# Kernel optimization log

Measured on AMD Instinct MI355X. Metric: run time of the kernel, lower is better.

Reference implementation:

```python
import jax, jax.numpy as jnp
from jax import lax
import numpy as np

BATCH = 8
INPUT_LEN = 768
OUTPUT_LEN = 192
MULTISCALE = (1, 2, 4)
HIDDEN = 256          # HiPPO order N == spectral channels
MODES = 32            # min(32, min(output_len, input_len)//2)
NUM_FEAT = 64


def hippo_matrices(N, dt):
    """HiPPO-LegT continuous matrices, bilinear-discretized (scipy cont2discrete equiv)."""
    Q = np.arange(N, dtype=np.float64)
    R = (2 * Q + 1)[:, None]
    j, i = np.meshgrid(Q, Q)
    A = np.where(i < j, -1.0, (-1.0) ** (i - j + 1)) * R
    B = ((-1.0) ** Q[:, None]) * R  # [N,1]
    I = np.eye(N)
    ima = I - (dt / 2.0) * A
    Ad = np.linalg.solve(ima, I + (dt / 2.0) * A)
    Bd = np.linalg.solve(ima, B * dt).squeeze(-1)
    return Ad.astype(np.float32), Bd.astype(np.float32)


def legendre_eval_matrix(N, dt):
    """eval_matrix[t, n] = P_n(1 - 2*vals[t]), vals = arange(0,1,dt)."""
    vals = np.arange(0.0, 1.0, dt)
    x = 1.0 - 2.0 * vals
    P = np.zeros((N, len(vals)), dtype=np.float64)
    P[0] = 1.0
    if N > 1:
        P[1] = x
    for n in range(1, N - 1):
        P[n + 1] = ((2 * n + 1) * x * P[n] - n * P[n - 1]) / (n + 1)
    return P.T.astype(np.float32)  # [len(vals), N]


def setup_inputs() -> dict:
    key = jax.random.key(0)
    k1, k2, k3, k4 = jax.random.split(key, 4)
    scale = 1.0 / (HIDDEN * HIDDEN)
    return {
        "inputs": jax.random.normal(k1, (BATCH, INPUT_LEN, NUM_FEAT), jnp.float32),
        "spec_wr": scale * jax.random.uniform(k2, (3, HIDDEN, HIDDEN, MODES), jnp.float32),
        "spec_wi": scale * jax.random.uniform(k3, (3, HIDDEN, HIDDEN, MODES), jnp.float32),
        "mlp_w": 0.1 * jax.random.normal(k4, (1, 3), jnp.float32),
        "mlp_b": jnp.zeros((1,), jnp.float32),
    }


def _film_forward(inputs, spec_wr, spec_wi, mlp_w, mlp_b):
    B_, _, D = inputs.shape
    preds = []
    for idx, scale in enumerate(MULTISCALE):
        dt = 1.0 / OUTPUT_LEN / scale
        Ad_np, Bd_np = hippo_matrices(HIDDEN, dt)
        em_np = legendre_eval_matrix(HIDDEN, dt)[-OUTPUT_LEN:]  # [out_len, N]
        Ad = jnp.asarray(Ad_np)
        Bd = jnp.asarray(Bd_np)
        em = jnp.asarray(em_np)
        T = scale * OUTPUT_LEN
        # HiPPO recurrence: c_t = c_{t-1} @ A^T + f_t * B  (sequential scan over time)
        f = jnp.transpose(inputs[:, -T:], (1, 0, 2))  # [T, B, D]

        def step(c, f_t, Ad=Ad, Bd=Bd):
            c = c @ Ad.T + f_t[..., None] * Bd
            return c, c

        c0 = jnp.zeros((B_, D, HIDDEN), inputs.dtype)
        _, cs = lax.scan(step, c0, f)               # [T, B, D, N]
        x = jnp.transpose(cs, (1, 2, 3, 0))          # [B, D, N, T]
        # SpectralConv1d: rfft -> complex mixing on low modes -> irfft
        x_ft = jnp.fft.rfft(x)                       # [B, D, N, T//2+1]
        w = (spec_wr[idx] + 1j * spec_wi[idx]).astype(jnp.complex64)  # [N, N, modes]
        out_m = jnp.einsum('bjix,iox->bjox', x_ft[..., :MODES], w)    # [B, D, N, modes]
        nfreq = T // 2 + 1
        out_ft = jnp.concatenate(
            [out_m, jnp.zeros(out_m.shape[:-1] + (nfreq - MODES,), out_m.dtype)], axis=-1)
        x = jnp.fft.irfft(out_ft, n=T)               # [B, D, N, T]
        # input_len >= output_len -> pick time index output_len-1, then project with Legendre
        x_out = x[:, :, :, OUTPUT_LEN - 1]           # [B, D, N]
        preds.append(x_out @ em.T)                   # [B, D, out_len]
    pred = jnp.stack(preds, axis=-1)                 # [B, D, out_len, 3]
    pred = jnp.squeeze(pred @ mlp_w.T + mlp_b, -1)   # [B, D, out_len]
    return jnp.transpose(pred, (0, 2, 1))            # [B, out_len, D]


def reference(inputs, spec_wr, spec_wi, mlp_w, mlp_b):
    return _film_forward(inputs, spec_wr, spec_wi, mlp_w, mlp_b)
```

## Files before the change

### kernel.cpp

```cpp
#include <hip/hip_runtime.h>


#define OFF_MF64  0
#define OFF_YA    1572864
#define OFF_YB    3145728
#define OFF_Z     4718592
#define OFF_F     7864320
#define OFF_PIV   8650752
#define OFF_FLAG  8653824
#define OFF_AP0   10223616
#define OFF_AP1   11010048
#define OFF_BD    11796480
#define OFF_V     11800576
#define OFF_EM    14159872
#define OFF_P     14749696
#define OFF_K     16125952
#define OFF_U4    29298688
#define OFF_WT4   117440512
#define OFF_C32   167772160
#define OFF_SEG4  211812352

typedef _Float16 half8 __attribute__((ext_vector_type(8)));
typedef float f32x4 __attribute__((ext_vector_type(4)));

__device__ __forceinline__ double a_entry(int i, int j){
  double base = (i < j) ? -1.0 : (((i - j) & 1) ? 1.0 : -1.0);
  return base * (double)(2*i + 1);
}

__device__ __forceinline__ unsigned int dpp_umax(unsigned int x){
  unsigned int t;
  t = (unsigned int)__builtin_amdgcn_update_dpp((int)x, (int)x, 0x111, 0xF, 0xF, false); x = x > t ? x : t;
  t = (unsigned int)__builtin_amdgcn_update_dpp((int)x, (int)x, 0x112, 0xF, 0xF, false); x = x > t ? x : t;
  t = (unsigned int)__builtin_amdgcn_update_dpp((int)x, (int)x, 0x114, 0xF, 0xE, false); x = x > t ? x : t;
  t = (unsigned int)__builtin_amdgcn_update_dpp((int)x, (int)x, 0x118, 0xF, 0xC, false); x = x > t ? x : t;
  t = (unsigned int)__builtin_amdgcn_update_dpp((int)x, (int)x, 0x142, 0xA, 0xF, false); x = x > t ? x : t;
  t = (unsigned int)__builtin_amdgcn_update_dpp((int)x, (int)x, 0x143, 0xC, 0xF, false); x = x > t ? x : t;
  return x;
}

__global__ void k_init(double* __restrict__ Mf64, float* __restrict__ em,
                       int* __restrict__ flags){
  int s = blockIdx.y, i = blockIdx.x, j = threadIdx.x;
  if (i < 256){
    double dt = (1.0 / 192.0) / (double)(1 << s);
    double m = ((i == j) ? 1.0 : 0.0) - 0.5 * dt * a_entry(i, j);
    Mf64[((size_t)s*256 + i)*256 + j] = m;
  } else {
    if (j < 192){
      int T = 192 << s;
      double dt = (1.0 / 192.0) / (double)(1 << s);
      double x = 1.0 - 2.0 * ((double)(T - 192 + j) * dt);
      float* row = em + ((size_t)s*192 + j)*256;
      double p0 = 1.0, p1 = x;
      row[0] = 1.0f; row[1] = (float)x;
      for (int n = 1; n < 255; ++n){
        double p2 = ((double)(2*n+1) * x * p1 - (double)n * p0) / (double)(n+1);
        row[n+1] = (float)p2;
        p0 = p1; p1 = p2;
      }
    } else if (j < 200){
      flags[s*8 + (j - 192)] = 0;
    }
  }
}

__global__ __launch_bounds__(256) void k_gj(float* __restrict__ Cg,
                                            int* __restrict__ pivg,
                                            int* __restrict__ flags,
                                            double* __restrict__ Ya){
  int s = blockIdx.x >> 4;
  int g = blockIdx.x & 15;
  int r = threadIdx.x;
  int c0 = g*32;
  float trow[32];
  if (g < 8){
    double dt = (1.0 / 192.0) / (double)(1 << s);
    #pragma unroll
    for (int j = 0; j < 32; ++j){
      int col = c0 + j;
      trow[j] = (float)(((r == col) ? 1.0 : 0.0) - 0.5*dt*a_entry(r, col));
    }
  } else {
    #pragma unroll
    for (int j = 0; j < 32; ++j) trow[j] = (r == c0 - 256 + j) ? 1.f : 0.f;
  }
  __shared__ float yl[32][32];
  __shared__ int pvs[32];
  __shared__ int pivAll[256];
  __shared__ float prow1[64];
  __shared__ unsigned int wv[4];
  __shared__ int invp[256];
  int used = 0;
  int* flagS = flags + s*8;
  int nrep = (g < 8) ? g : 8;

  for (int kp = 0; kp < nrep; ++kp){
    if (r == 0){
      int cnt = 0;
      while (__hip_atomic_load(&flagS[kp], __ATOMIC_ACQUIRE, __HIP_MEMORY_SCOPE_AGENT) == 0){
        __builtin_amdgcn_s_sleep(2);
        if (++cnt > 100000000) break;
      }
    }
    __syncthreads();
    if (r < 32){
      int p = pivg[s*256 + kp*32 + r];
      pvs[r] = p;
      if (g >= 8) pivAll[kp*32 + r] = p;
    }
    float cp[32];
    const float* Cr = Cg + ((size_t)(s*8 + kp))*8192 + r*32;
    #pragma unroll
    for (int l = 0; l < 32; l += 4){
      float4 v = *(const float4*)&Cr[l];
      cp[l] = v.x; cp[l+1] = v.y; cp[l+2] = v.z; cp[l+3] = v.w;
    }
    __syncthreads();
    if (g < 8){
      #pragma unroll
      for (int l = 0; l < 32; ++l) if (pvs[l] == r) used = 1;
    }
    #pragma unroll
    for (int l = 0; l < 32; ++l){
      if (pvs[l] == r){
        #pragma unroll
        for (int j = 0; j < 32; ++j) yl[l][j] = trow[j];
      }
    }
    __syncthreads();
    #pragma unroll
    for (int l = 0; l < 32; ++l){
      float y[32];
      #pragma unroll
      for (int j = 0; j < 32; j += 4){
        float4 v = *(const float4*)&yl[l][j];
        y[j] = v.x; y[j+1] = v.y; y[j+2] = v.z; y[j+3] = v.w;
      }
      float c = cp[l];
      #pragma unroll
      for (int j = 0; j < 32; ++j) trow[j] += c * y[j];
    }
  }

  if (g < 8){
    float xrow[32];
    #pragma unroll
    for (int l = 0; l < 32; ++l) xrow[l] = 0.f;
    #pragma unroll
    for (int l = 0; l < 32; ++l){
      float av = fabsf(trow[l]);
      unsigned int kb = __builtin_bit_cast(unsigned int, av);
      unsigned int key = used ? 0u : ((kb & 0xFFFFFF00u) | (unsigned int)(255 - r));
      key = dpp_umax(key);
      if ((r & 63) == 63) wv[r >> 6] = key;
      __syncthreads();
      unsigned int b0 = wv[0] > wv[1] ? wv[0] : wv[1];
      unsigned int b1 = wv[2] > wv[3] ? wv[2] : wv[3];
      unsigned int best = b0 > b1 ? b0 : b1;
      int piv = 255 - (int)(best & 0xFFu);
      if (r == piv){
        float inv = 1.0f / trow[l];
        used = 1;
        xrow[l] = 1.0f;
        #pragma unroll
        for (int j = 0; j < 32; ++j){ trow[j] *= inv; prow1[j] = trow[j]; }
        #pragma unroll
        for (int m = 0; m < 32; ++m){ xrow[m] *= inv; prow1[32 + m] = xrow[m]; }
      }
      if (r == 0) pvs[l] = piv;
      __syncthreads();
      if (r != piv){
        float f = trow[l];
        #pragma unroll
        for (int j = 0; j < 32; ++j) trow[j] -= f * prow1[j];
        #pragma unroll
        for (int m = 0; m < 32; ++m) xrow[m] -= f * prow1[32 + m];
      }
    }
    float* Cw = Cg + ((size_t)(s*8 + g))*8192 + r*32;
    #pragma unroll
    for (int l = 0; l < 32; ++l)
      Cw[l] = xrow[l] - ((pvs[l] == r) ? 1.0f : 0.0f);
    if (r < 32) pivg[s*256 + g*32 + r] = pvs[r];
    __threadfence();
    __syncthreads();
    if (r == 0)
      __hip_atomic_store(&flagS[g], 1, __ATOMIC_RELEASE, __HIP_MEMORY_SCOPE_AGENT);
  } else {
    invp[pivAll[r]] = r;
    __syncthreads();
    int dst = invp[r];
    double* Yr = Ya + ((size_t)s*256 + dst)*256 + (c0 - 256);
    #pragma unroll
    for (int j = 0; j < 32; ++j) Yr[j] = (double)trow[j];
  }
}

__global__ void k_mmZ(const double* __restrict__ M, const double* __restrict__ Y,
                      double* __restrict__ Z){
  int s = blockIdx.y;
  const double* A = M + (size_t)s*65536;
  const double* B = Y + (size_t)s*65536;
  int c = threadIdx.x, r0 = blockIdx.x * 8;
  double acc[8] = {0,0,0,0,0,0,0,0};
  for (int j = 0; j < 256; ++j){
    double b = B[(size_t)j*256 + c];
    #pragma unroll
    for (int q = 0; q < 8; ++q) acc[q] += A[(size_t)(r0+q)*256 + j] * b;
  }
  #pragma unroll
  for (int q = 0; q < 8; ++q) Z[(size_t)s*65536 + (size_t)(r0+q)*256 + c] = acc[q];
}

__global__ void k_mmN(const double* __restrict__ Y, const double* __restrict__ Z,
                      double* __restrict__ Yn){
  int s = blockIdx.y;
  const double* A = Y + (size_t)s*65536;
  const double* B = Z + (size_t)s*65536;
  int c = threadIdx.x, r0 = blockIdx.x * 8;
  double acc[8] = {0,0,0,0,0,0,0,0};
  for (int j = 0; j < 256; ++j){
    double b = B[(size_t)j*256 + c];
    #pragma unroll
    for (int q = 0; q < 8; ++q) acc[q] += A[(size_t)(r0+q)*256 + j] * b;
  }
  #pragma unroll
  for (int q = 0; q < 8; ++q)
    Yn[(size_t)s*65536 + (size_t)(r0+q)*256 + c] =
      2.0 * A[(size_t)(r0+q)*256 + c] - acc[q];
}

__global__ void k_final(const double* __restrict__ Y, float* __restrict__ Ad,
                        float* __restrict__ Bd, float* __restrict__ V){
  int s = blockIdx.y;
  const double* Ys = Y + (size_t)s*65536;
  if (blockIdx.x < 64){
    int c = threadIdx.x, r0 = blockIdx.x * 4;
    #pragma unroll
    for (int q = 0; q < 4; ++q){
      double v = 2.0 * Ys[(size_t)(r0+q)*256 + c] - ((r0+q) == c ? 1.0 : 0.0);
      Ad[(size_t)s*65536 + (size_t)(r0+q)*256 + c] = (float)v;
    }
  } else {
    int i = threadIdx.x;
    double dt = (1.0 / 192.0) / (double)(1 << s);
    double acc = 0.0;
    for (int j = 0; j < 256; ++j){
      double bj = dt * ((j & 1) ? -1.0 : 1.0) * (double)(2*j + 1);
      acc += Ys[(size_t)i*256 + j] * bj;
    }
    float b = (float)acc;
    Bd[s*256 + i] = b;
    V[((size_t)s*768 + 0)*256 + i] = b;
  }
}

__global__ void k_level(const float* __restrict__ Pin, float* __restrict__ Pout,
                        float* __restrict__ V, int L, int noSquare){
  int s = blockIdx.y;
  const float* A = Pin + (size_t)s*65536;
  int bx = blockIdx.x;
  if (bx < 64){
    if (noSquare) return;
    int c = threadIdx.x, r0 = bx * 4;
    float acc[4] = {0,0,0,0};
    for (int k = 0; k < 256; ++k){
      float b = A[(size_t)k*256 + c];
      #pragma unroll
      for (int q = 0; q < 4; ++q) acc[q] += A[(size_t)(r0+q)*256 + k] * b;
    }
    #pragma unroll
    for (int q = 0; q < 4; ++q) Pout[(size_t)s*65536 + (size_t)(r0+q)*256 + c] = acc[q];
  } else {
    int j = threadIdx.x;
    if (j >= L || L + j >= 768) return;
    int r0 = (bx - 64) * 4;
    float* Vs = V + (size_t)s*768*256;
    float acc[4] = {0,0,0,0};
    for (int k = 0; k < 256; ++k){
      float v = Vs[(size_t)j*256 + k];
      #pragma unroll
      for (int q = 0; q < 4; ++q) acc[q] += A[(size_t)(r0+q)*256 + k] * v;
    }
    #pragma unroll
    for (int q = 0; q < 4; ++q) Vs[(size_t)(L+j)*256 + r0 + q] = acc[q];
  }
}

__global__ void k_wt(const float* __restrict__ wr, const float* __restrict__ wi,
                     float* __restrict__ Wt4){
  int s = blockIdx.x, i = blockIdx.y, tid = threadIdx.x;
  size_t srcbase = ((size_t)s*256 + i)*256;
  float* dst = Wt4 + ((size_t)s*256 + i)*16384;
  for (int ph = 0; ph < 64; ++ph){
    int col = ph*256 + tid;
    int kl = col >> 9, ri = (col >> 8) & 1, o = col & 255;
    const float* src = ri ? wi : wr;
    dst[col] = src[(srcbase + o)*32 + kl];
  }
}

__device__ __forceinline__ void splitf16(float x, unsigned short &h, unsigned short &l){
  _Float16 hf = (_Float16)x;
  _Float16 lf = (_Float16)(x - (float)hf);
  h = __builtin_bit_cast(unsigned short, hf);
  l = __builtin_bit_cast(unsigned short, lf);
}
__device__ __forceinline__ unsigned int pk(unsigned short a, unsigned short b){
  return (unsigned int)a | ((unsigned int)b << 16);
}

__global__ __launch_bounds__(256) void k_ugemm(const float* __restrict__ V,
                                               const float* __restrict__ Wt4,
                                               float* __restrict__ U){
  int s = blockIdx.z;
  int Ts = 192 << s;
  int mt = blockIdx.y;
  if (mt*64 >= Ts) return;
  int nb = blockIdx.x * 64;
  const float* Vs = V + (size_t)s*768*256;
  const float* Bm = Wt4 + (size_t)s*256*16384;
  __shared__ unsigned int Ah[4*65*4], Al[4*65*4];
  __shared__ unsigned int Bh[4*65*4], Bl[4*65*4];
  int tid = threadIdx.x;
  int lane = tid & 63;
  int w = tid >> 6;
  int m0 = (w >> 1) * 32, n0 = (w & 1) * 32;
  int ml = lane & 15, quad = lane >> 4;
  f32x4 acc[2][2];
  #pragma unroll
  for (int t = 0; t < 2; ++t)
    #pragma unroll
    for (int u = 0; u < 2; ++u) acc[t][u] = (f32x4){0.f,0.f,0.f,0.f};

  int am = tid >> 2, akf = tid & 3;
  int bn = tid & 63, bq = tid >> 6;

  for (int kk = 0; kk < 8; ++kk){
    if (kk) __syncthreads();
    {
      const float* ap = &Vs[(size_t)(mt*64 + am)*256 + kk*32 + akf*8];
      float4 a0 = *(const float4*)ap;
      float4 a1 = *(const float4*)(ap + 4);
      unsigned short h[8], l[8];
      splitf16(a0.x*16.f, h[0], l[0]); splitf16(a0.y*16.f, h[1], l[1]);
      splitf16(a0.z*16.f, h[2], l[2]); splitf16(a0.w*16.f, h[3], l[3]);
      splitf16(a1.x*16.f, h[4], l[4]); splitf16(a1.y*16.f, h[5], l[5]);
      splitf16(a1.z*16.f, h[6], l[6]); splitf16(a1.w*16.f, h[7], l[7]);
      int base = (akf*65 + am)*4;
      *(uint4*)&Ah[base] = make_uint4(pk(h[0],h[1]), pk(h[2],h[3]), pk(h[4],h[5]), pk(h[6],h[7]));
      *(uint4*)&Al[base] = make_uint4(pk(l[0],l[1]), pk(l[2],l[3]), pk(l[4],l[5]), pk(l[6],l[7]));
    }
    {
      unsigned short h[8], l[8];
      #pragma unroll
      for (int j = 0; j < 8; ++j){
        float b = Bm[(size_t)(kk*32 + bq*8 + j)*16384 + nb + bn];
        splitf16(b*65536.f, h[j], l[j]);
      }
      int base = (bq*65 + bn)*4;
      *(uint4*)&Bh[base] = make_uint4(pk(h[0],h[1]), pk(h[2],h[3]), pk(h[4],h[5]), pk(h[6],h[7]));
      *(uint4*)&Bl[base] = make_uint4(pk(l[0],l[1]), pk(l[2],l[3]), pk(l[4],l[5]), pk(l[6],l[7]));
    }
    __syncthreads();
    half8 ah[2], al[2], bh[2], bl[2];
    #pragma unroll
    for (int t = 0; t < 2; ++t){
      int idx = (quad*65 + m0 + 16*t + ml)*4;
      ah[t] = *(const half8*)&Ah[idx];
      al[t] = *(const half8*)&Al[idx];
    }
    #pragma unroll
    for (int u = 0; u < 2; ++u){
      int idx = (quad*65 + n0 + 16*u + ml)*4;
      bh[u] = *(const half8*)&Bh[idx];
      bl[u] = *(const half8*)&Bl[idx];
    }
    #pragma unroll
    for (int t = 0; t < 2; ++t)
      #pragma unroll
      for (int u = 0; u < 2; ++u){
        acc[t][u] = __builtin_amdgcn_mfma_f32_16x16x32_f16(ah[t], bh[u], acc[t][u], 0, 0, 0);
        acc[t][u] = __builtin_amdgcn_mfma_f32_16x16x32_f16(ah[t], bl[u], acc[t][u], 0, 0, 0);
        acc[t][u] = __builtin_amdgcn_mfma_f32_16x16x32_f16(al[t], bh[u], acc[t][u], 0, 0, 0);
      }
  }
  int ub = (s == 0) ? 0 : (s == 1 ? 192 : 576);
  const float unscale = 1.0f / 1048576.0f;
  #pragma unroll
  for (int t = 0; t < 2; ++t)
    #pragma unroll
    for (int u = 0; u < 2; ++u){
      int row = ub + mt*64 + m0 + 16*t + quad*4;
      int col = nb + n0 + 16*u + ml;
      #pragma unroll
      for (int r = 0; r < 4; ++r)
        U[(size_t)(row + r)*16384 + col] = acc[t][u][r] * unscale;
    }
}

__global__ void k_scanA(float* __restrict__ U, float* __restrict__ Seg){
  int seg = blockIdx.x;
  int kl  = blockIdx.y;
  int s   = blockIdx.z;
  int k = kl;
  int T = 192 << s;
  int Ls = T >> 3;
  int m0 = seg * Ls;
  int ub = (s == 0) ? 0 : (s == 1 ? 192 : 576);
  int o = threadIdx.x;
  float* Ur = U + ((size_t)(ub + m0))*16384 + kl*512 + o;
  float th = 6.283185307179586f / (float)T;
  int im = (k * m0) % T;
  float Zr = 0.f, Zi = 0.f;
  #pragma unroll 4
  for (int i = 0; i < Ls; ++i){
    float ur = Ur[0];
    float ui = Ur[256];
    float sa, ca; __sincosf(th * (float)im, &sa, &ca);
    Zr += ca*ur + sa*ui;
    Zi += ca*ui - sa*ur;
    Ur[0] = Zr; Ur[256] = Zi;
    im += k; if (im >= T) im -= T;
    Ur += 16384;
  }
  float* Sg = Seg + (((size_t)(s*32 + kl)*8 + seg)*2)*256 + o;
  Sg[0] = Zr; Sg[256] = Zi;
}

__global__ void k_scanC(const float* __restrict__ U, const float* __restrict__ Seg,
                        float* __restrict__ C32){
  int seg = blockIdx.x, kl = blockIdx.y, s = blockIdx.z;
  int k = kl;
  int T = 192 << s;
  int Ls = T >> 3;
  int m0 = seg * Ls;
  int ub = (s == 0) ? 0 : (s == 1 ? 192 : 576);
  int o = threadIdx.x;
  float offr = 0.f, offi = 0.f;
  const float* Sg = Seg + ((size_t)(s*32 + kl)*8)*512 + o;
  for (int j = 0; j < seg; ++j){ offr += Sg[(size_t)j*512]; offi += Sg[(size_t)j*512 + 256]; }
  const float* Ur = U + ((size_t)(ub + m0))*16384 + kl*512 + o;
  float* Cb = C32 + ((size_t)kl*1344 + ub)*256 + o;
  float ckT = ((k == 0) ? 1.0f : 2.0f) / (float)T;
  float th = 6.283185307179586f / (float)T;
  int ib = (k * (192 + m0)) % T;
  #pragma unroll 4
  for (int i = 0; i < Ls; ++i){
    int m = m0 + i;
    float zr = offr + Ur[0];
    float zi = offi + Ur[256];
    float sb, cb; __sincosf(th * (float)ib, &sb, &cb);
    Cb[(size_t)(T-1-m)*256] = ckT * (zr*cb - zi*sb);
    ib += k; if (ib >= T) ib -= T;
    Ur += 16384;
  }
}

__global__ void k_reduce(const float* __restrict__ C32, float* __restrict__ P){
  int row = blockIdx.x;
  int o = threadIdx.x;
  float a = 0.f;
  #pragma unroll
  for (int kl = 0; kl < 32; ++kl) a += C32[((size_t)kl*1344 + row)*256 + o];
  P[(size_t)row*256 + o] = a;
}

__global__ __launch_bounds__(256) void k_K(const float* __restrict__ em,
                                           const float* __restrict__ P,
                                           const float* __restrict__ mlpw,
                                           float* __restrict__ K){
  int tn = blockIdx.x;
  int tmb = blockIdx.y;
  __shared__ float Es[16][68];
  __shared__ float Ps[16][68];
  int tid = threadIdx.x;
  int tm = tid >> 4, tnn = tid & 15;
  int srow = tid >> 2;
  int acol4 = (tid & 3) * 4;
  float acc[4][4];
  #pragma unroll
  for (int a = 0; a < 4; ++a)
    #pragma unroll
    for (int b = 0; b < 4; ++b) acc[a][b] = 0.f;
  for (int s = 0; s < 3; ++s){
    int T = 192 << s;
    int off = 768 - T;
    if (tn*64 < off) continue;
    int ub = (s == 0) ? 0 : (s == 1 ? 192 : 576);
    float mw = mlpw[s];
    const float* ems = em + ((size_t)s*192 + tmb*64)*256;
    const float* Pb = P + ((size_t)ub + (tn*64 - off))*256;
    float sacc[4][4];
    #pragma unroll
    for (int a = 0; a < 4; ++a)
      #pragma unroll
      for (int b = 0; b < 4; ++b) sacc[a][b] = 0.f;
    for (int k0 = 0; k0 < 256; k0 += 16){
      float4 e4 = *(const float4*)&ems[(size_t)srow*256 + k0 + acol4];
      Es[acol4+0][srow] = e4.x; Es[acol4+1][srow] = e4.y;
      Es[acol4+2][srow] = e4.z; Es[acol4+3][srow] = e4.w;
      float4 p4 = *(const float4*)&Pb[(size_t)srow*256 + k0 + acol4];
      Ps[acol4+0][srow] = p4.x; Ps[acol4+1][srow] = p4.y;
      Ps[acol4+2][srow] = p4.z; Ps[acol4+3][srow] = p4.w;
      __syncthreads();
      #pragma unroll
      for (int k = 0; k < 16; ++k){
        float av[4], bv[4];
        *(float4*)av = *(const float4*)&Es[k][tm*4];
        *(float4*)bv = *(const float4*)&Ps[k][tnn*4];
        #pragma unroll
        for (int a = 0; a < 4; ++a)
          #pragma unroll
          for (int b = 0; b < 4; ++b) sacc[a][b] += av[a]*bv[b];
      }
      __syncthreads();
    }
    #pragma unroll
    for (int a = 0; a < 4; ++a)
      #pragma unroll
      for (int b = 0; b < 4; ++b) acc[a][b] += mw * sacc[a][b];
  }
  int to0 = tmb*64 + tm*4;
  int tg0 = tn*64 + tnn*4;
  #pragma unroll
  for (int a = 0; a < 4; ++a){
    float4 o4 = make_float4(acc[a][0], acc[a][1], acc[a][2], acc[a][3]);
    *(float4*)&K[(size_t)(to0+a)*768 + tg0] = o4;
  }
}

__global__ __launch_bounds__(256) void k_out(const float* __restrict__ K,
                                             const float* __restrict__ inp,
                                             const float* __restrict__ mlpb,
                                             float* __restrict__ out){
  int to = blockIdx.x, b = blockIdx.y;
  int d = threadIdx.x & 63;
  int w = threadIdx.x >> 6;
  const float* Kr = K + (size_t)to*768 + w*192;
  const float* ip = inp + (size_t)b*768*64 + (size_t)(w*192)*64 + d;
  float acc = 0.f;
  #pragma unroll 4
  for (int i = 0; i < 192; ++i) acc += Kr[i] * ip[(size_t)i*64];
  __shared__ float red[4][64];
  red[w][d] = acc;
  __syncthreads();
  if (w == 0)
    out[((size_t)b*192 + to)*64 + d] =
      red[0][d] + red[1][d] + red[2][d] + red[3][d] + mlpb[0];
}

extern "C" void kernel_launch(void* const* d_in, const int* in_sizes, int n_in,
                              void* d_out, int out_size, void* d_ws, size_t ws_size,
                              hipStream_t stream){
  const float* inputs  = (const float*)d_in[0];
  const float* spec_wr = (const float*)d_in[1];
  const float* spec_wi = (const float*)d_in[2];
  const float* mlp_w   = (const float*)d_in[3];
  const float* mlp_b   = (const float*)d_in[4];
  float* out = (float*)d_out;
  char* ws = (char*)d_ws;

  double* Mf64 = (double*)(ws + OFF_MF64);
  double* Ya   = (double*)(ws + OFF_YA);
  double* Yb   = (double*)(ws + OFF_YB);
  double* Zb   = (double*)(ws + OFF_Z);
  float* Cg   = (float*)(ws + OFF_F);
  int*   pivg = (int*)(ws + OFF_PIV);
  int*   flags= (int*)(ws + OFF_FLAG);
  float* AP0  = (float*)(ws + OFF_AP0);
  float* AP1  = (float*)(ws + OFF_AP1);
  float* Bd   = (float*)(ws + OFF_BD);
  float* V    = (float*)(ws + OFF_V);
  float* em   = (float*)(ws + OFF_EM);
  float* P    = (float*)(ws + OFF_P);
  float* Km   = (float*)(ws + OFF_K);
  float* U4   = (float*)(ws + OFF_U4);
  float* Wt4  = (float*)(ws + OFF_WT4);
  float* C32  = (float*)(ws + OFF_C32);
  float* Seg4 = (float*)(ws + OFF_SEG4);

  k_init<<<dim3(257,3), 256, 0, stream>>>(Mf64, em, flags);
  k_gj<<<48, 256, 0, stream>>>(Cg, pivg, flags, Ya);
  for (int it = 0; it < 2; ++it){
    double* yi = (it & 1) ? Yb : Ya;
    double* yo = (it & 1) ? Ya : Yb;
    k_mmZ<<<dim3(32,3), 256, 0, stream>>>(Mf64, yi, Zb);
    k_mmN<<<dim3(32,3), 256, 0, stream>>>(yi, Zb, yo);
  }
  k_final<<<dim3(65,3), 256, 0, stream>>>(Ya, AP0, Bd, V);

  float* pin = AP0; float* pout = AP1;
  for (int L = 1; L <= 512; L <<= 1){
    k_level<<<dim3(128,3), 256, 0, stream>>>(pin, pout, V, L, (L == 512) ? 1 : 0);
    float* t = pin; pin = pout; pout = t;
  }

  k_wt<<<dim3(3,256), 256, 0, stream>>>(spec_wr, spec_wi, Wt4);
  k_ugemm<<<dim3(256,12,3), 256, 0, stream>>>(V, Wt4, U4);
  k_scanA<<<dim3(8,32,3), 256, 0, stream>>>(U4, Seg4);
  k_scanC<<<dim3(8,32,3), 256, 0, stream>>>(U4, Seg4, C32);
  k_reduce<<<1344, 256, 0, stream>>>(C32, P);
  k_K<<<dim3(12,3), 256, 0, stream>>>(em, P, mlp_w, Km);
  k_out<<<dim3(192,8), 256, 0, stream>>>(Km, inputs, mlp_b, out);
}
```

Before: 860.0 us.

## Run panel pivot elimination in a single wavefront via shared memory

The 32-column panel factorization moves out of per-thread registers into a shared-memory panel and is done by one 64-lane wavefront, each lane owning four rows. This removes the two block-wide barriers per pivot step and the cross-wave max reduction, using a readlane instead. The stored C matrix layout changes to column-major to fit the panel, and the spin-wait sleep interval is raised. The cost is fewer active threads doing the row updates and more shared-memory traffic.

```diff
diff --git a/kernel.cpp b/kernel.cpp
--- a/kernel.cpp
+++ b/kernel.cpp
@@ -85,11 +85,10 @@
     #pragma unroll
     for (int j = 0; j < 32; ++j) trow[j] = (r == c0 - 256 + j) ? 1.f : 0.f;
   }
+  __shared__ float B[32*256];
   __shared__ float yl[32][32];
   __shared__ int pvs[32];
   __shared__ int pivAll[256];
-  __shared__ float prow1[64];
-  __shared__ unsigned int wv[4];
   __shared__ int invp[256];
   int used = 0;
   int* flagS = flags + s*8;
@@ -99,7 +98,7 @@
     if (r == 0){
       int cnt = 0;
       while (__hip_atomic_load(&flagS[kp], __ATOMIC_ACQUIRE, __HIP_MEMORY_SCOPE_AGENT) == 0){
-        __builtin_amdgcn_s_sleep(2);
+        __builtin_amdgcn_s_sleep(8);
         if (++cnt > 100000000) break;
       }
     }
@@ -110,12 +109,9 @@
       if (g >= 8) pivAll[kp*32 + r] = p;
     }
     float cp[32];
-    const float* Cr = Cg + ((size_t)(s*8 + kp))*8192 + r*32;
-    #pragma unroll
-    for (int l = 0; l < 32; l += 4){
-      float4 v = *(const float4*)&Cr[l];
-      cp[l] = v.x; cp[l+1] = v.y; cp[l+2] = v.z; cp[l+3] = v.w;
-    }
+    const float* Cr = Cg + ((size_t)(s*8 + kp))*8192;
+    #pragma unroll
+    for (int l = 0; l < 32; ++l) cp[l] = Cr[l*256 + r];
     __syncthreads();
     if (g < 8){
       #pragma unroll
@@ -141,51 +137,79 @@
       #pragma unroll
       for (int j = 0; j < 32; ++j) trow[j] += c * y[j];
     }
+    __syncthreads();
   }
 
   if (g < 8){
-    float xrow[32];
-    #pragma unroll
-    for (int l = 0; l < 32; ++l) xrow[l] = 0.f;
-    #pragma unroll
+    #pragma unroll
+    for (int c = 0; c < 32; ++c) B[c*256 + r] = trow[c];
+    pivAll[r] = used;
+    __syncthreads();
+    if (r >= 64) return;
+    int lane = r;
+    int usedq[4];
+    #pragma unroll
+    for (int q = 0; q < 4; ++q) usedq[q] = pivAll[q*64 + lane];
+
+    #pragma unroll 1
     for (int l = 0; l < 32; ++l){
-      float av = fabsf(trow[l]);
-      unsigned int kb = __builtin_bit_cast(unsigned int, av);
-      unsigned int key = used ? 0u : ((kb & 0xFFFFFF00u) | (unsigned int)(255 - r));
+      float f4[4];
+      unsigned int key = 0;
+      #pragma unroll
+      for (int q = 0; q < 4; ++q){
+        int row = q*64 + lane;
+        float v = B[l*256 + row];
+        f4[q] = v;
+        unsigned int kb = __builtin_bit_cast(unsigned int, fabsf(v));
+        unsigned int k2 = usedq[q] ? 0u : ((kb & 0xFFFFFF00u) | (unsigned int)(255 - row));
+        key = key > k2 ? key : k2;
+      }
       key = dpp_umax(key);
-      if ((r & 63) == 63) wv[r >> 6] = key;
-      __syncthreads();
-      unsigned int b0 = wv[0] > wv[1] ? wv[0] : wv[1];
-      unsigned int b1 = wv[2] > wv[3] ? wv[2] : wv[3];
-      unsigned int best = b0 > b1 ? b0 : b1;
+      unsigned int best = (unsigned int)__builtin_amdgcn_readlane((int)key, 63);
       int piv = 255 - (int)(best & 0xFFu);
-      if (r == piv){
-        float inv = 1.0f / trow[l];
-        used = 1;
-        xrow[l] = 1.0f;
-        #pragma unroll
-        for (int j = 0; j < 32; ++j){ trow[j] *= inv; prow1[j] = trow[j]; }
-        #pragma unroll
-        for (int m = 0; m < 32; ++m){ xrow[m] *= inv; prow1[32 + m] = xrow[m]; }
-      }
-      if (r == 0) pvs[l] = piv;
-      __syncthreads();
-      if (r != piv){
-        float f = trow[l];
-        #pragma unroll
-        for (int j = 0; j < 32; ++j) trow[j] -= f * prow1[j];
-        #pragma unroll
-        for (int m = 0; m < 32; ++m) xrow[m] -= f * prow1[32 + m];
-      }
-    }
-    float* Cw = Cg + ((size_t)(s*8 + g))*8192 + r*32;
-    #pragma unroll
-    for (int l = 0; l < 32; ++l)
-      Cw[l] = xrow[l] - ((pvs[l] == r) ? 1.0f : 0.0f);
-    if (r < 32) pivg[s*256 + g*32 + r] = pvs[r];
+      float pv = B[l*256 + piv];
+      float inv = 1.0f / pv;
+      #pragma unroll
+      for (int q = 0; q < 4; ++q){
+        if (q*64 + lane == piv) usedq[q] = 1;
+        if (q*64 + lane == piv) f4[q] = 0.f;
+      }
+      if (lane < 32){
+        float nv = (lane == l) ? inv : B[lane*256 + piv] * inv;
+        B[lane*256 + piv] = nv;
+      }
+      #pragma unroll
+      for (int c = 0; c < 32; ++c){
+        float pr = B[c*256 + piv];
+        if (c == l){
+          #pragma unroll
+          for (int q = 0; q < 4; ++q){
+            int row = q*64 + lane;
+            B[c*256 + row] = (row == piv) ? pr : -f4[q]*pr;
+          }
+        } else {
+          #pragma unroll
+          for (int q = 0; q < 4; ++q){
+            int row = q*64 + lane;
+            B[c*256 + row] -= f4[q]*pr;
+          }
+        }
+      }
+      if (lane == 0) pvs[l] = piv;
+    }
+    float* Cw = Cg + ((size_t)(s*8 + g))*8192;
+    #pragma unroll 1
+    for (int l = 0; l < 32; ++l){
+      int p = pvs[l];
+      #pragma unroll
+      for (int q = 0; q < 4; ++q){
+        int row = q*64 + lane;
+        Cw[l*256 + row] = B[l*256 + row] - ((row == p) ? 1.0f : 0.0f);
+      }
+    }
+    if (lane < 32) pivg[s*256 + g*32 + lane] = pvs[lane];
     __threadfence();
-    __syncthreads();
-    if (r == 0)
+    if (lane == 0)
       __hip_atomic_store(&flagS[g], 1, __ATOMIC_RELEASE, __HIP_MEMORY_SCOPE_AGENT);
   } else {
     invp[pivAll[r]] = r;
```

New measurement: 1.394 ms. +62.1%, slower.
